# Kernel optimization log

Measured on AMD Instinct MI355X. Metric: run time of the kernel, lower is better.

Reference implementation:

```python
import jax, jax.numpy as jnp
import numpy as np

D_MODEL = 1024
N_HEADS = 16
HEAD_DIM = D_MODEL // N_HEADS
B, T_Q, T_CACHE = 2, 2048, 2048


def setup_inputs() -> dict:
    key = jax.random.key(0)
    ks = jax.random.split(key, 12)
    s = 1.0 / np.sqrt(D_MODEL)
    return {
        "x": jax.random.normal(ks[0], (B, T_Q, D_MODEL), jnp.float32),
        "k_cache": jax.random.normal(ks[1], (B, N_HEADS, T_CACHE, HEAD_DIM), jnp.float32),
        "v_cache": jax.random.normal(ks[2], (B, N_HEADS, T_CACHE, HEAD_DIM), jnp.float32),
        "Wq": jax.random.normal(ks[3], (D_MODEL, D_MODEL), jnp.float32) * s,
        "bq": jax.random.normal(ks[4], (D_MODEL,), jnp.float32) * s,
        "Wk": jax.random.normal(ks[5], (D_MODEL, D_MODEL), jnp.float32) * s,
        "bk": jax.random.normal(ks[6], (D_MODEL,), jnp.float32) * s,
        "Wv": jax.random.normal(ks[7], (D_MODEL, D_MODEL), jnp.float32) * s,
        "bv": jax.random.normal(ks[8], (D_MODEL,), jnp.float32) * s,
        "Wo": jax.random.normal(ks[9], (D_MODEL, D_MODEL), jnp.float32) * s,
        "bo": jax.random.normal(ks[10], (D_MODEL,), jnp.float32) * s,
    }


def reference(x, k_cache, v_cache, Wq, bq, Wk, bk, Wv, bv, Wo, bo):
    B_, T, C = x.shape
    H, Dh = N_HEADS, HEAD_DIM
    scale = Dh ** -0.5

    def proj(W, b):
        # [B,T,C] -> [B,H,T,Dh]
        y = jnp.einsum('btc,cd->btd', x, W) + b
        return y.reshape(B_, T, H, Dh).transpose(0, 2, 1, 3)

    q = proj(Wq, bq)
    k = jnp.concatenate([k_cache, proj(Wk, bk)], axis=2)
    v = jnp.concatenate([v_cache, proj(Wv, bv)], axis=2)

    Tq, Tk = q.shape[2], k.shape[2]
    scores = jnp.einsum('bhqd,bhkd->bhqk', q, k) * scale  # [B,H,Tq,Tk]
    # causal: query i attends to keys j <= i + (Tk - Tq)
    i = jnp.arange(Tq)[:, None]
    j = jnp.arange(Tk)[None, :]
    mask = j > i + (Tk - Tq)
    scores = jnp.where(mask, -jnp.inf, scores)
    attn = jax.nn.softmax(scores, axis=-1)
    out = jnp.einsum('bhqk,bhkd->bhqd', attn, v)
    out = out.transpose(0, 2, 1, 3).reshape(B_, T, C)
    out = jnp.einsum('btc,cd->btd', out, Wo) + bo
    return out, (k, v)
```

## Files before the change

### kernel.cpp

```cpp
#include <hip/hip_runtime.h>
#include <hip/hip_bf16.h>
#include <cstdint>
#include <cstddef>

#define DM 1024
#define NH 16
#define DH 64
#define BB 2
#define TQ 2048
#define TCACHE 2048
#define TKTOT 4096
#define MROWS 4096

typedef __attribute__((ext_vector_type(8))) short bf16x8;
typedef __attribute__((ext_vector_type(4))) short bf16x4;
typedef __attribute__((ext_vector_type(4))) float f32x4;
typedef __attribute__((ext_vector_type(16))) float f32x16;

__device__ __forceinline__ unsigned pk2(float a, float b) {
  unsigned r;
  asm("v_cvt_pk_bf16_f32 %0, %1, %2" : "=v"(r) : "v"(a), "v"(b));
  return r;
}

__device__ __forceinline__ short f2bf(float f) {
  return (short)(unsigned short)pk2(f, f);
}

__device__ __forceinline__ uint2 pk4(float x, float y, float z, float w) {
  uint2 r;
  r.x = pk2(x, y);
  r.y = pk2(z, w);
  return r;
}

__device__ __forceinline__ float bf2f(short s) {
  union { unsigned u; float f; } v;
  v.u = ((unsigned)(unsigned short)s) << 16;
  return v.f;
}

__device__ __forceinline__ float exp2fast(float x) {
#if __has_builtin(__builtin_amdgcn_exp2f)
  return __builtin_amdgcn_exp2f(x);
#else
  return exp2f(x);
#endif
}

__device__ __forceinline__ void plswap(unsigned& a, unsigned& b) {
  asm volatile("v_permlane32_swap_b32 %0, %1" : "+v"(a), "+v"(b));
}

__device__ __forceinline__ void gld_lds16(const short* g, short* l) {
  __builtin_amdgcn_global_load_lds(
      (const __attribute__((address_space(1))) void*)((uintptr_t)g),
      (__attribute__((address_space(3))) void*)((uintptr_t)l), 16, 0, 0);
}

__global__ __launch_bounds__(256) void k_prep(
    const float* __restrict__ x, short* __restrict__ xb,
    const float* __restrict__ W0, const float* __restrict__ W1,
    const float* __restrict__ W2, const float* __restrict__ W3,
    short* __restrict__ Wt,
    const float* __restrict__ kc, short* __restrict__ Kb,
    const float* __restrict__ vc, short* __restrict__ Vtb) {
  __shared__ short lds[64 * 65];
  const int bid = (int)blockIdx.x;
  if (bid < 4096) {
    const size_t i = (size_t)bid * 256 + threadIdx.x;
    const float4 v = ((const float4*)x)[i];
    *(uint2*)(((short4*)xb) + i) = pk4(v.x, v.y, v.z, v.w);
  } else if (bid < 8192) {
    const int local = bid - 4096;
    const int bx = local & 31, by = (local >> 5) & 31, bz = local >> 10;
    short (*tile)[33] = (short(*)[33])lds;
    const float* W = (bz == 0) ? W0 : (bz == 1) ? W1 : (bz == 2) ? W2 : W3;
    short* dst = Wt + (size_t)bz * DM * DM;
    const int k0 = by * 32, n0 = bx * 32;
    const int tx = threadIdx.x & 31, ty = threadIdx.x >> 5;
#pragma unroll
    for (int r = 0; r < 4; r++) {
      const int k = ty + r * 8;
      tile[k][tx] = f2bf(W[(size_t)(k0 + k) * DM + n0 + tx]);
    }
    __syncthreads();
#pragma unroll
    for (int r = 0; r < 4; r++) {
      const int n = ty + r * 8;
      dst[(size_t)(n0 + n) * DM + k0 + tx] = tile[tx][n];
    }
  } else if (bid < 12288) {
    const size_t i = (size_t)(bid - 8192) * 256 + threadIdx.x;
    const float4 v = ((const float4*)kc)[i];
    const size_t e = i * 4;
    const int dh = (int)(e & 63);
    const int t = (int)((e >> 6) & 2047);
    const int bh = (int)(e >> 17);
    *(uint2*)(Kb + ((size_t)bh * TKTOT + t) * DH + dh) = pk4(v.x, v.y, v.z, v.w);
  } else {
    const int local = bid - 12288;
    const int bh = local >> 5;
    const int t0 = (local & 31) * 64;
    short (*tile)[65] = (short(*)[65])lds;
    const int tx = threadIdx.x & 15, ty = threadIdx.x >> 4;
    const float* src = vc + ((size_t)bh * TCACHE + t0) * DH;
#pragma unroll
    for (int r = 0; r < 4; r++) {
      const int t = ty + r * 16;
      const float4 v = *(const float4*)(src + (size_t)t * DH + tx * 4);
      tile[tx * 4 + 0][t] = f2bf(v.x);
      tile[tx * 4 + 1][t] = f2bf(v.y);
      tile[tx * 4 + 2][t] = f2bf(v.z);
      tile[tx * 4 + 3][t] = f2bf(v.w);
    }
    __syncthreads();
    short* vt = Vtb + (size_t)bh * DH * TKTOT + t0;
#pragma unroll
    for (int r = 0; r < 4; r++) {
      const int dh = ty + r * 16;
      short4 o;
      o.x = tile[dh][tx * 4 + 0];
      o.y = tile[dh][tx * 4 + 1];
      o.z = tile[dh][tx * 4 + 2];
      o.w = tile[dh][tx * 4 + 3];
      *(short4*)(vt + (size_t)dh * TKTOT + tx * 4) = o;
    }
  }
}

__global__ __launch_bounds__(256) void k_gemm(
    const short* __restrict__ A, const short* __restrict__ Bt,
    const float* __restrict__ b0, const float* __restrict__ b1, const float* __restrict__ b2,
    const int is_qkv, float* __restrict__ fdst,
    short* __restrict__ Qb, short* __restrict__ Kb, short* __restrict__ Vtb) {
  const int z = is_qkv ? (int)blockIdx.z : 3;
  const short* Bz = Bt + (is_qkv ? (size_t)z * DM * DM : 0);
  const float* bias = (z == 0 || z == 3) ? b0 : (z == 1 ? b1 : b2);

  __shared__ short sA[2][128 * 32];
  __shared__ short sB[2][128 * 32];

  const int m0 = blockIdx.y * 128;
  const int n0 = blockIdx.x * 128;
  const int tid = threadIdx.x;
  const int wv = tid >> 6;
  const int lane = tid & 63;
  const int quad = lane >> 4;
  const int l16 = lane & 15;
  const int wm = (wv >> 1) * 64;
  const int wn = (wv & 1) * 64;

  const f32x4 zero = {0.f, 0.f, 0.f, 0.f};
  f32x4 acc[4][4];
#pragma unroll
  for (int i = 0; i < 4; i++)
#pragma unroll
    for (int j = 0; j < 4; j++) acc[i][j] = zero;

  const int sw = (quad ^ ((l16 >> 1) & 3)) << 4;
  const int afo = (wm + l16) * 64 + sw;
  const int bfo = (wn + l16) * 64 + sw;

#define STAGEG(k0_, b_)                                                         \
  do {                                                                          \
    _Pragma("unroll") for (int s = 0; s < 2; s++) {                             \
      const int c = tid + s * 256;                                              \
      const int row = c >> 2, cs = c & 3;                                       \
      const int gc = cs ^ ((row >> 1) & 3);                                     \
      gld_lds16(A + (size_t)(m0 + row) * DM + (k0_) + gc * 8, &sA[b_][c * 8]);  \
      gld_lds16(Bz + (size_t)(n0 + row) * DM + (k0_) + gc * 8, &sB[b_][c * 8]); \
    }                                                                           \
  } while (0)

  STAGEG(0, 0);
  __syncthreads();
  int buf = 0;
  for (int k0 = 0; k0 < DM; k0 += 32) {
    if (k0 + 32 < DM) STAGEG(k0 + 32, buf ^ 1);
    const char* Ab = (const char*)&sA[0][0] + buf * 8192;
    const char* Bb = (const char*)&sB[0][0] + buf * 8192;
    bf16x8 af[4], bfv[4];
#pragma unroll
    for (int i = 0; i < 4; i++) af[i] = *(const bf16x8*)(Ab + afo + i * 1024);
#pragma unroll
    for (int j = 0; j < 4; j++) bfv[j] = *(const bf16x8*)(Bb + bfo + j * 1024);
    __builtin_amdgcn_s_setprio(1);
#pragma unroll
    for (int i = 0; i < 4; i++)
#pragma unroll
      for (int j = 0; j < 4; j++)
        acc[i][j] = __builtin_amdgcn_mfma_f32_16x16x32_bf16(af[i], bfv[j], acc[i][j], 0, 0, 0);
    __builtin_amdgcn_s_setprio(0);
    __syncthreads();
    buf ^= 1;
  }
#undef STAGEG

#pragma unroll
  for (int i = 0; i < 4; i++) {
#pragma unroll
    for (int j = 0; j < 4; j++) {
      const int gn = n0 + wn + j * 16 + l16;
      const float bb = bias[gn];
#pragma unroll
      for (int r = 0; r < 4; r++) {
        const int gm = m0 + wm + i * 16 + quad * 4 + r;
        const float v = acc[i][j][r] + bb;
        if (z == 3) {
          fdst[(size_t)gm * DM + gn] = v;
        } else {
          const int b_ = gm >> 11, t = gm & 2047;
          const int h_ = gn >> 6, dh = gn & 63;
          if (z == 0) {
            Qb[(((size_t)(b_ * NH + h_)) * TQ + t) * DH + dh] = f2bf(v * 0.18033688011f);
          } else if (z == 1) {
            Kb[(((size_t)(b_ * NH + h_)) * TKTOT + TCACHE + t) * DH + dh] = f2bf(v);
          } else {
            Vtb[(((size_t)(b_ * NH + h_)) * DH + dh) * TKTOT + TCACHE + t] = f2bf(v);
          }
        }
      }
    }
  }
}

__global__ __launch_bounds__(256, 4) void k_attn(const short* __restrict__ Qb,
                                                 const short* __restrict__ Kb,
                                                 const short* __restrict__ Vtb,
                                                 float* __restrict__ Opart,
                                                 float* __restrict__ Lpart) {
  __shared__ short sK[2][64 * 64];
  __shared__ short sV[2][64 * 64];

  const int split = (int)blockIdx.x;
  const int qx = 15 - (int)blockIdx.y;
  const int bh = (int)blockIdx.z;
  const int q0 = qx * 128;
  const int tid = threadIdx.x;
  const int wq = tid >> 6;
  const int lane = tid & 63;
  const int l32 = lane & 31;
  const int h = lane >> 5;

  const int nkt = 2 * qx + 34;
  const int kt0 = (nkt * split) >> 2;
  const int kt1 = (nkt * (split + 1)) >> 2;

  const short* Kg = Kb + (size_t)bh * TKTOT * DH;
  const short* Vtg = Vtb + (size_t)bh * DH * TKTOT;

  const int c0 = tid, c1 = tid + 256;
  const int r0 = c0 >> 3, g0 = ((c0 & 7) ^ (r0 & 7)) * 8;
  const int r1 = c1 >> 3, g1 = ((c1 & 7) ^ (r1 & 7)) * 8;
  const short* Kst0 = Kg + (size_t)r0 * DH + g0;
  const short* Kst1 = Kg + (size_t)r1 * DH + g1;
  const short* Vst0 = Vtg + (size_t)r0 * TKTOT + g0;
  const short* Vst1 = Vtg + (size_t)r1 * TKTOT + g1;

  const short* Qrow = Qb + ((size_t)bh * TQ + q0 + wq * 32 + l32) * DH;
  bf16x8 qf[4];
#pragma unroll
  for (int s = 0; s < 4; s++) qf[s] = *(const bf16x8*)(Qrow + s * 16 + h * 8);

  const char* sKc = (const char*)&sK[0][0];
  const char* sVc = (const char*)&sV[0][0];
  const int rx7 = l32 & 7;
  const int base0 = l32 * 128;
  const int base1 = base0 + 4096;
  int co[4];
#pragma unroll
  for (int ks = 0; ks < 4; ks++) co[ks] = ((2 * ks + h) ^ rx7) << 4;

  const f32x16 zerov = {0, 0, 0, 0, 0, 0, 0, 0, 0, 0, 0, 0, 0, 0, 0, 0};
  f32x16 of0 = zerov;
  f32x16 of1 = zerov;
  float la = 0.f, lb = 0.f, lc = 0.f, ld = 0.f;

#define STAGE(t_, b_)                               \
  do {                                              \
    const size_t koff = (size_t)(t_) * 64 * DH;     \
    const size_t voff = (size_t)(t_) * 64;          \
    short* dK = &sK[b_][0];                         \
    short* dV = &sV[b_][0];                         \
    gld_lds16(Kst0 + koff, dK + c0 * 8);            \
    gld_lds16(Kst1 + koff, dK + c1 * 8);            \
    gld_lds16(Vst0 + voff, dV + c0 * 8);            \
    gld_lds16(Vst1 + voff, dV + c1 * 8);            \
  } while (0)

  STAGE(kt0, 0);
  __syncthreads();
  int buf = 0;

  for (int t = kt0; t < kt1; t++) {
    if (t + 1 < kt1) STAGE(t + 1, buf ^ 1);
    const char* kb_ = sKc + buf * 8192;
    const char* vb_ = sVc + buf * 8192;

    f32x16 sacc0, sacc1;
    __builtin_amdgcn_s_setprio(1);
    {
      const bf16x8 kf0 = *(const bf16x8*)(kb_ + base0 + co[0]);
      const bf16x8 kf1 = *(const bf16x8*)(kb_ + base1 + co[0]);
      sacc0 = __builtin_amdgcn_mfma_f32_32x32x16_bf16(kf0, qf[0], zerov, 0, 0, 0);
      sacc1 = __builtin_amdgcn_mfma_f32_32x32x16_bf16(kf1, qf[0], zerov, 0, 0, 0);
    }
#pragma unroll
    for (int ks = 1; ks < 4; ks++) {
      const bf16x8 kf0 = *(const bf16x8*)(kb_ + base0 + co[ks]);
      const bf16x8 kf1 = *(const bf16x8*)(kb_ + base1 + co[ks]);
      sacc0 = __builtin_amdgcn_mfma_f32_32x32x16_bf16(kf0, qf[ks], sacc0, 0, 0, 0);
      sacc1 = __builtin_amdgcn_mfma_f32_32x32x16_bf16(kf1, qf[ks], sacc1, 0, 0, 0);
    }
    __builtin_amdgcn_s_setprio(0);

    if (t >= nkt - 2) {
      const int qgl = q0 + wq * 32 + l32 + TCACHE;
      const int kb0 = t * 64 + 4 * h;
#pragma unroll
      for (int r = 0; r < 16; r++) {
        const int key = kb0 + (r & 3) + 8 * (r >> 2);
        if (key > qgl) sacc0[r] = -1e30f;
        if (key + 32 > qgl) sacc1[r] = -1e30f;
      }
    }
#pragma unroll
    for (int r = 0; r < 16; r++) {
      const float e0 = exp2fast(sacc0[r]);
      const float e1 = exp2fast(sacc1[r]);
      sacc0[r] = e0;
      sacc1[r] = e1;
      if ((r & 3) == 0) la += e0 + e1;
      else if ((r & 3) == 1) lb += e0 + e1;
      else if ((r & 3) == 2) lc += e0 + e1;
      else ld += e0 + e1;
    }

    bf16x8 pa[4];
#pragma unroll
    for (int s = 0; s < 4; s++) {
      const int o = (s & 1) * 8;
      unsigned w0, w1, w2, w3;
      if (s < 2) {
        w0 = pk2(sacc0[o + 0], sacc0[o + 1]);
        w1 = pk2(sacc0[o + 2], sacc0[o + 3]);
        w2 = pk2(sacc0[o + 4], sacc0[o + 5]);
        w3 = pk2(sacc0[o + 6], sacc0[o + 7]);
      } else {
        w0 = pk2(sacc1[o + 0], sacc1[o + 1]);
        w1 = pk2(sacc1[o + 2], sacc1[o + 3]);
        w2 = pk2(sacc1[o + 4], sacc1[o + 5]);
        w3 = pk2(sacc1[o + 6], sacc1[o + 7]);
      }
      plswap(w0, w2);
      plswap(w1, w3);
      union { unsigned u[4]; bf16x8 v; } pu;
      pu.u[0] = w0; pu.u[1] = w1; pu.u[2] = w2; pu.u[3] = w3;
      pa[s] = pu.v;
    }

    __builtin_amdgcn_s_setprio(1);
#pragma unroll
    for (int ks = 0; ks < 4; ks++) {
      const bf16x8 vf0 = *(const bf16x8*)(vb_ + base0 + co[ks]);
      const bf16x8 vf1 = *(const bf16x8*)(vb_ + base1 + co[ks]);
      of0 = __builtin_amdgcn_mfma_f32_32x32x16_bf16(pa[ks], vf0, of0, 0, 0, 0);
      of1 = __builtin_amdgcn_mfma_f32_32x32x16_bf16(pa[ks], vf1, of1, 0, 0, 0);
    }
    __builtin_amdgcn_s_setprio(0);
    __syncthreads();
    buf ^= 1;
  }
#undef STAGE

  const int pid = (bh * 16 + qx) * 4 + split;
  float* Op = Opart + (size_t)pid * 8192;
#pragma unroll
  for (int r = 0; r < 16; r++) {
    const int ql = wq * 32 + (r & 3) + 8 * (r >> 2) + 4 * h;
    Op[ql * 64 + l32] = of0[r];
    Op[ql * 64 + 32 + l32] = of1[r];
  }
  const float l_lane = (la + lb) + (lc + ld);
  const float l_tot = l_lane + __shfl_xor(l_lane, 32);
  if (h == 0) Lpart[(size_t)pid * 128 + wq * 32 + l32] = l_tot;
}

__global__ __launch_bounds__(256) void k_reduce(const float* __restrict__ Opart,
                                                const float* __restrict__ Lpart,
                                                short* __restrict__ AOb) {
  const int qx = (int)blockIdx.x, bh = (int)blockIdx.y;
  const int b = bh >> 4, hd = bh & 15;
  const int qxb = qx >> 1, hf = qx & 1;
  const int pid = (bh * 16 + qxb) * 4;
  const float* Ob = Opart + (size_t)pid * 8192 + hf * 4096;
  const int t = threadIdx.x;
  const int r_ = t >> 2, c4 = t & 3;
  float l = 0.f;
#pragma unroll
  for (int s = 0; s < 4; s++) l += Lpart[(size_t)(pid + s) * 128 + hf * 64 + r_];
  const float inv = 1.f / l;
  short* dst = AOb + ((size_t)(b * TQ + qx * 64 + r_)) * DM + hd * 64 + c4 * 16;
#pragma unroll
  for (int u = 0; u < 4; u++) {
    const int off = r_ * 64 + c4 * 16 + u * 4;
    float4 a = *(const float4*)(Ob + off);
#pragma unroll
    for (int s = 1; s < 4; s++) {
      const float4 v = *(const float4*)(Ob + (size_t)s * 8192 + off);
      a.x += v.x; a.y += v.y; a.z += v.z; a.w += v.w;
    }
    *(uint2*)(dst + u * 4) = pk4(a.x * inv, a.y * inv, a.z * inv, a.w * inv);
  }
}

__global__ __launch_bounds__(256) void k_expand(const float* __restrict__ kc,
                                                const short* __restrict__ Kb,
                                                float* __restrict__ kF,
                                                const float* __restrict__ vc,
                                                const short* __restrict__ Vtb,
                                                float* __restrict__ vF) {
  __shared__ short tile[64 * 72];
  const int bid = (int)blockIdx.x;
  if (bid < 8192) {
    const size_t f4 = (size_t)bid * 256 + threadIdx.x;
    const size_t e = f4 * 4;
    const int t = (int)((e >> 6) & 4095);
    float4 v;
    if (t < TCACHE) {
      const int dh = (int)(e & 63);
      const int bh = (int)(e >> 18);
      v = *(const float4*)(kc + ((size_t)(bh * TCACHE + t)) * DH + dh);
    } else {
      const short4 s = *(const short4*)(Kb + e);
      v.x = bf2f(s.x); v.y = bf2f(s.y); v.z = bf2f(s.z); v.w = bf2f(s.w);
    }
    *(float4*)(kF + e) = v;
  } else {
    const int local = bid - 8192;
    const int tt = local & 63, bh = local >> 6;
    if (tt < 32) {
#pragma unroll
      for (int k2 = 0; k2 < 4; k2++) {
        const int f = threadIdx.x + k2 * 256;
        const int trow = f >> 4, dh4 = f & 15;
        const size_t si = ((size_t)(bh * TCACHE) + tt * 64 + trow) * DH + dh4 * 4;
        const size_t di = ((size_t)(bh * TKTOT) + tt * 64 + trow) * DH + dh4 * 4;
        *(float4*)(vF + di) = *(const float4*)(vc + si);
      }
    } else {
      const int t0 = tt * 64;
#pragma unroll
      for (int k2 = 0; k2 < 4; k2++) {
        const int f = threadIdx.x + k2 * 256;
        const int dh = f >> 4, tc4 = f & 15;
        const short4 s = *(const short4*)(Vtb + ((size_t)(bh * DH + dh)) * TKTOT + t0 + tc4 * 4);
        *(short4*)(&tile[dh * 72 + tc4 * 4]) = s;
      }
      __syncthreads();
#pragma unroll
      for (int k2 = 0; k2 < 4; k2++) {
        const int f = threadIdx.x + k2 * 256;
        const int trow = f >> 4, dh4 = f & 15;
        float4 v;
        v.x = bf2f(tile[(dh4 * 4 + 0) * 72 + trow]);
        v.y = bf2f(tile[(dh4 * 4 + 1) * 72 + trow]);
        v.z = bf2f(tile[(dh4 * 4 + 2) * 72 + trow]);
        v.w = bf2f(tile[(dh4 * 4 + 3) * 72 + trow]);
        *(float4*)(vF + ((size_t)(bh * TKTOT) + t0 + trow) * DH + dh4 * 4) = v;
      }
    }
  }
}


extern "C" void kernel_launch(void* const* d_in, const int* in_sizes, int n_in,
                              void* d_out, int out_size, void* d_ws, size_t ws_size,
                              hipStream_t stream) {
  const float* x = (const float*)d_in[0];
  const float* kc = (const float*)d_in[1];
  const float* vc = (const float*)d_in[2];
  const float* Wq = (const float*)d_in[3];
  const float* bq = (const float*)d_in[4];
  const float* Wk = (const float*)d_in[5];
  const float* bk = (const float*)d_in[6];
  const float* Wv = (const float*)d_in[7];
  const float* bv = (const float*)d_in[8];
  const float* Wo = (const float*)d_in[9];
  const float* bo = (const float*)d_in[10];

  float* out = (float*)d_out;
  float* kF = out + (size_t)BB * TQ * DM;
  float* vF = kF + (size_t)BB * NH * TKTOT * DH;
  float* Opart = kF;
  float* Lpart = out;

  char* ws = (char*)d_ws;
  short* xb = (short*)ws;   ws += (size_t)MROWS * DM * 2;
  short* Wt = (short*)ws;   ws += (size_t)4 * DM * DM * 2;
  short* Qb = (short*)ws;   ws += (size_t)BB * NH * TQ * DH * 2;
  short* Kb = (short*)ws;   ws += (size_t)BB * NH * TKTOT * DH * 2;
  short* Vtb = (short*)ws;  ws += (size_t)BB * NH * TKTOT * DH * 2;
  short* AOb = (short*)ws;

  k_prep<<<13312, 256, 0, stream>>>(x, xb, Wq, Wk, Wv, Wo, Wt, kc, Kb, vc, Vtb);
  k_gemm<<<dim3(DM / 128, MROWS / 128, 3), 256, 0, stream>>>(
      xb, Wt, bq, bk, bv, 1, nullptr, Qb, Kb, Vtb);
  k_attn<<<dim3(4, 16, 32), 256, 0, stream>>>(Qb, Kb, Vtb, Opart, Lpart);
  k_reduce<<<dim3(32, 32), 256, 0, stream>>>(Opart, Lpart, AOb);
  k_expand<<<10240, 256, 0, stream>>>(kc, Kb, kF, vc, Vtb, vF);
  k_gemm<<<dim3(DM / 128, MROWS / 128, 1), 256, 0, stream>>>(
      AOb, Wt + (size_t)3 * DM * DM, bo, bo, bo, 0, out, nullptr, nullptr, nullptr);
}
```

Baseline: 317.0 us.

## Fuse attention, reduction and KV expansion into one kernel without split-K

Removes the 4-way key split of the attention kernel, so each block handles all key tiles for its query tile and normalizes and writes bf16 output directly. This drops the partial-output buffers and the separate reduce kernel. The KV-cache fp32 expansion is merged into the same launch as extra blocks that can fill idle CUs while long attention blocks run. Attention blocks are ordered to interleave long and short causal tiles. The trade-off is fewer, longer attention blocks (512 instead of 2048), which raises tail imbalance risk in exchange for one fewer launch and less partial-sum traffic.

```diff
diff --git a/kernel.cpp b/kernel.cpp
--- a/kernel.cpp
+++ b/kernel.cpp
@@ -225,206 +225,170 @@
   }
 }
 
-__global__ __launch_bounds__(256, 4) void k_attn(const short* __restrict__ Qb,
-                                                 const short* __restrict__ Kb,
-                                                 const short* __restrict__ Vtb,
-                                                 float* __restrict__ Opart,
-                                                 float* __restrict__ Lpart) {
-  __shared__ short sK[2][64 * 64];
-  __shared__ short sV[2][64 * 64];
-
-  const int split = (int)blockIdx.x;
-  const int qx = 15 - (int)blockIdx.y;
-  const int bh = (int)blockIdx.z;
-  const int q0 = qx * 128;
-  const int tid = threadIdx.x;
-  const int wq = tid >> 6;
-  const int lane = tid & 63;
-  const int l32 = lane & 31;
-  const int h = lane >> 5;
-
-  const int nkt = 2 * qx + 34;
-  const int kt0 = (nkt * split) >> 2;
-  const int kt1 = (nkt * (split + 1)) >> 2;
-
-  const short* Kg = Kb + (size_t)bh * TKTOT * DH;
-  const short* Vtg = Vtb + (size_t)bh * DH * TKTOT;
-
-  const int c0 = tid, c1 = tid + 256;
-  const int r0 = c0 >> 3, g0 = ((c0 & 7) ^ (r0 & 7)) * 8;
-  const int r1 = c1 >> 3, g1 = ((c1 & 7) ^ (r1 & 7)) * 8;
-  const short* Kst0 = Kg + (size_t)r0 * DH + g0;
-  const short* Kst1 = Kg + (size_t)r1 * DH + g1;
-  const short* Vst0 = Vtg + (size_t)r0 * TKTOT + g0;
-  const short* Vst1 = Vtg + (size_t)r1 * TKTOT + g1;
-
-  const short* Qrow = Qb + ((size_t)bh * TQ + q0 + wq * 32 + l32) * DH;
-  bf16x8 qf[4];
-#pragma unroll
-  for (int s = 0; s < 4; s++) qf[s] = *(const bf16x8*)(Qrow + s * 16 + h * 8);
-
-  const char* sKc = (const char*)&sK[0][0];
-  const char* sVc = (const char*)&sV[0][0];
-  const int rx7 = l32 & 7;
-  const int base0 = l32 * 128;
-  const int base1 = base0 + 4096;
-  int co[4];
-#pragma unroll
-  for (int ks = 0; ks < 4; ks++) co[ks] = ((2 * ks + h) ^ rx7) << 4;
-
-  const f32x16 zerov = {0, 0, 0, 0, 0, 0, 0, 0, 0, 0, 0, 0, 0, 0, 0, 0};
-  f32x16 of0 = zerov;
-  f32x16 of1 = zerov;
-  float la = 0.f, lb = 0.f, lc = 0.f, ld = 0.f;
-
-#define STAGE(t_, b_)                               \
-  do {                                              \
-    const size_t koff = (size_t)(t_) * 64 * DH;     \
-    const size_t voff = (size_t)(t_) * 64;          \
-    short* dK = &sK[b_][0];                         \
-    short* dV = &sV[b_][0];                         \
-    gld_lds16(Kst0 + koff, dK + c0 * 8);            \
-    gld_lds16(Kst1 + koff, dK + c1 * 8);            \
-    gld_lds16(Vst0 + voff, dV + c0 * 8);            \
-    gld_lds16(Vst1 + voff, dV + c1 * 8);            \
-  } while (0)
-
-  STAGE(kt0, 0);
-  __syncthreads();
-  int buf = 0;
-
-  for (int t = kt0; t < kt1; t++) {
-    if (t + 1 < kt1) STAGE(t + 1, buf ^ 1);
-    const char* kb_ = sKc + buf * 8192;
-    const char* vb_ = sVc + buf * 8192;
-
-    f32x16 sacc0, sacc1;
-    __builtin_amdgcn_s_setprio(1);
-    {
-      const bf16x8 kf0 = *(const bf16x8*)(kb_ + base0 + co[0]);
-      const bf16x8 kf1 = *(const bf16x8*)(kb_ + base1 + co[0]);
-      sacc0 = __builtin_amdgcn_mfma_f32_32x32x16_bf16(kf0, qf[0], zerov, 0, 0, 0);
-      sacc1 = __builtin_amdgcn_mfma_f32_32x32x16_bf16(kf1, qf[0], zerov, 0, 0, 0);
-    }
-#pragma unroll
-    for (int ks = 1; ks < 4; ks++) {
-      const bf16x8 kf0 = *(const bf16x8*)(kb_ + base0 + co[ks]);
-      const bf16x8 kf1 = *(const bf16x8*)(kb_ + base1 + co[ks]);
-      sacc0 = __builtin_amdgcn_mfma_f32_32x32x16_bf16(kf0, qf[ks], sacc0, 0, 0, 0);
-      sacc1 = __builtin_amdgcn_mfma_f32_32x32x16_bf16(kf1, qf[ks], sacc1, 0, 0, 0);
-    }
-    __builtin_amdgcn_s_setprio(0);
-
-    if (t >= nkt - 2) {
-      const int qgl = q0 + wq * 32 + l32 + TCACHE;
-      const int kb0 = t * 64 + 4 * h;
+__global__ __launch_bounds__(256, 4) void k_attn_expand(
+    const short* __restrict__ Qb, const short* __restrict__ Kb,
+    const short* __restrict__ Vtb, short* __restrict__ AOb,
+    const float* __restrict__ kc, float* __restrict__ kF,
+    const float* __restrict__ vc, float* __restrict__ vF) {
+  __shared__ short SH[16384];
+
+  const int bid = (int)blockIdx.x;
+  if (bid < 512) {
+    const int y = bid >> 5;
+    const int bh = bid & 31;
+    const int qx = (y < 8) ? (15 - y) : (y - 8);
+    const int q0 = qx * 128;
+    const int tid = threadIdx.x;
+    const int wq = tid >> 6;
+    const int lane = tid & 63;
+    const int l32 = lane & 31;
+    const int h = lane >> 5;
+
+    const int nkt = 2 * qx + 34;
+
+    const short* Kg = Kb + (size_t)bh * TKTOT * DH;
+    const short* Vtg = Vtb + (size_t)bh * DH * TKTOT;
+
+    const int c0 = tid, c1 = tid + 256;
+    const int r0 = c0 >> 3, g0 = ((c0 & 7) ^ (r0 & 7)) * 8;
+    const int r1 = c1 >> 3, g1 = ((c1 & 7) ^ (r1 & 7)) * 8;
+    const short* Kst0 = Kg + (size_t)r0 * DH + g0;
+    const short* Kst1 = Kg + (size_t)r1 * DH + g1;
+    const short* Vst0 = Vtg + (size_t)r0 * TKTOT + g0;
+    const short* Vst1 = Vtg + (size_t)r1 * TKTOT + g1;
+
+    const short* Qrow = Qb + ((size_t)bh * TQ + q0 + wq * 32 + l32) * DH;
+    bf16x8 qf[4];
+#pragma unroll
+    for (int s = 0; s < 4; s++) qf[s] = *(const bf16x8*)(Qrow + s * 16 + h * 8);
+
+    const char* sKc = (const char*)SH;
+    const char* sVc = (const char*)SH + 16384;
+    const int rx7 = l32 & 7;
+    const int base0 = l32 * 128;
+    const int base1 = base0 + 4096;
+    int co[4];
+#pragma unroll
+    for (int ks = 0; ks < 4; ks++) co[ks] = ((2 * ks + h) ^ rx7) << 4;
+
+    const f32x16 zerov = {0, 0, 0, 0, 0, 0, 0, 0, 0, 0, 0, 0, 0, 0, 0, 0};
+    f32x16 of0 = zerov;
+    f32x16 of1 = zerov;
+    float la = 0.f, lb = 0.f, lc = 0.f, ld = 0.f;
+
+#define STAGE(t_, b_)                                    \
+    do {                                                 \
+      const size_t koff = (size_t)(t_) * 64 * DH;        \
+      const size_t voff = (size_t)(t_) * 64;             \
+      short* dK = SH + (b_)*4096;                        \
+      short* dV = SH + 8192 + (b_)*4096;                 \
+      gld_lds16(Kst0 + koff, dK + c0 * 8);               \
+      gld_lds16(Kst1 + koff, dK + c1 * 8);               \
+      gld_lds16(Vst0 + voff, dV + c0 * 8);               \
+      gld_lds16(Vst1 + voff, dV + c1 * 8);               \
+    } while (0)
+
+    STAGE(0, 0);
+    __syncthreads();
+    int buf = 0;
+
+    for (int t = 0; t < nkt; t++) {
+      if (t + 1 < nkt) STAGE(t + 1, buf ^ 1);
+      const char* kb_ = sKc + buf * 8192;
+      const char* vb_ = sVc + buf * 8192;
+
+      f32x16 sacc0, sacc1;
+      __builtin_amdgcn_s_setprio(1);
+      {
+        const bf16x8 kf0 = *(const bf16x8*)(kb_ + base0 + co[0]);
+        const bf16x8 kf1 = *(const bf16x8*)(kb_ + base1 + co[0]);
+        sacc0 = __builtin_amdgcn_mfma_f32_32x32x16_bf16(kf0, qf[0], zerov, 0, 0, 0);
+        sacc1 = __builtin_amdgcn_mfma_f32_32x32x16_bf16(kf1, qf[0], zerov, 0, 0, 0);
+      }
+#pragma unroll
+      for (int ks = 1; ks < 4; ks++) {
+        const bf16x8 kf0 = *(const bf16x8*)(kb_ + base0 + co[ks]);
+        const bf16x8 kf1 = *(const bf16x8*)(kb_ + base1 + co[ks]);
+        sacc0 = __builtin_amdgcn_mfma_f32_32x32x16_bf16(kf0, qf[ks], sacc0, 0, 0, 0);
+        sacc1 = __builtin_amdgcn_mfma_f32_32x32x16_bf16(kf1, qf[ks], sacc1, 0, 0, 0);
+      }
+      __builtin_amdgcn_s_setprio(0);
+
+      if (t >= nkt - 2) {
+        const int qgl = q0 + wq * 32 + l32 + TCACHE;
+        const int kb0 = t * 64 + 4 * h;
+#pragma unroll
+        for (int r = 0; r < 16; r++) {
+          const int key = kb0 + (r & 3) + 8 * (r >> 2);
+          if (key > qgl) sacc0[r] = -1e30f;
+          if (key + 32 > qgl) sacc1[r] = -1e30f;
+        }
+      }
 #pragma unroll
       for (int r = 0; r < 16; r++) {
-        const int key = kb0 + (r & 3) + 8 * (r >> 2);
-        if (key > qgl) sacc0[r] = -1e30f;
-        if (key + 32 > qgl) sacc1[r] = -1e30f;
-      }
-    }
+        const float e0 = exp2fast(sacc0[r]);
+        const float e1 = exp2fast(sacc1[r]);
+        sacc0[r] = e0;
+        sacc1[r] = e1;
+        if ((r & 3) == 0) la += e0 + e1;
+        else if ((r & 3) == 1) lb += e0 + e1;
+        else if ((r & 3) == 2) lc += e0 + e1;
+        else ld += e0 + e1;
+      }
+
+      bf16x8 pa[4];
+#pragma unroll
+      for (int s = 0; s < 4; s++) {
+        const int o = (s & 1) * 8;
+        unsigned w0, w1, w2, w3;
+        if (s < 2) {
+          w0 = pk2(sacc0[o + 0], sacc0[o + 1]);
+          w1 = pk2(sacc0[o + 2], sacc0[o + 3]);
+          w2 = pk2(sacc0[o + 4], sacc0[o + 5]);
+          w3 = pk2(sacc0[o + 6], sacc0[o + 7]);
+        } else {
+          w0 = pk2(sacc1[o + 0], sacc1[o + 1]);
+          w1 = pk2(sacc1[o + 2], sacc1[o + 3]);
+          w2 = pk2(sacc1[o + 4], sacc1[o + 5]);
+          w3 = pk2(sacc1[o + 6], sacc1[o + 7]);
+        }
+        plswap(w0, w2);
+        plswap(w1, w3);
+        union { unsigned u[4]; bf16x8 v; } pu;
+        pu.u[0] = w0; pu.u[1] = w1; pu.u[2] = w2; pu.u[3] = w3;
+        pa[s] = pu.v;
+      }
+
+      __builtin_amdgcn_s_setprio(1);
+#pragma unroll
+      for (int ks = 0; ks < 4; ks++) {
+        const bf16x8 vf0 = *(const bf16x8*)(vb_ + base0 + co[ks]);
+        const bf16x8 vf1 = *(const bf16x8*)(vb_ + base1 + co[ks]);
+        of0 = __builtin_amdgcn_mfma_f32_32x32x16_bf16(pa[ks], vf0, of0, 0, 0, 0);
+        of1 = __builtin_amdgcn_mfma_f32_32x32x16_bf16(pa[ks], vf1, of1, 0, 0, 0);
+      }
+      __builtin_amdgcn_s_setprio(0);
+      __syncthreads();
+      buf ^= 1;
+    }
+#undef STAGE
+
+    float* sLf = (float*)SH;
+    const float l_lane = (la + lb) + (lc + ld);
+    const float l_tot = l_lane + __shfl_xor(l_lane, 32);
+    if (h == 0) sLf[wq * 32 + l32] = l_tot;
+    const int b_ = bh >> 4, h_ = bh & 15;
 #pragma unroll
     for (int r = 0; r < 16; r++) {
-      const float e0 = exp2fast(sacc0[r]);
-      const float e1 = exp2fast(sacc1[r]);
-      sacc0[r] = e0;
-      sacc1[r] = e1;
-      if ((r & 3) == 0) la += e0 + e1;
-      else if ((r & 3) == 1) lb += e0 + e1;
-      else if ((r & 3) == 2) lc += e0 + e1;
-      else ld += e0 + e1;
-    }
-
-    bf16x8 pa[4];
-#pragma unroll
-    for (int s = 0; s < 4; s++) {
-      const int o = (s & 1) * 8;
-      unsigned w0, w1, w2, w3;
-      if (s < 2) {
-        w0 = pk2(sacc0[o + 0], sacc0[o + 1]);
-        w1 = pk2(sacc0[o + 2], sacc0[o + 3]);
-        w2 = pk2(sacc0[o + 4], sacc0[o + 5]);
-        w3 = pk2(sacc0[o + 6], sacc0[o + 7]);
-      } else {
-        w0 = pk2(sacc1[o + 0], sacc1[o + 1]);
-        w1 = pk2(sacc1[o + 2], sacc1[o + 3]);
-        w2 = pk2(sacc1[o + 4], sacc1[o + 5]);
-        w3 = pk2(sacc1[o + 6], sacc1[o + 7]);
-      }
-      plswap(w0, w2);
-      plswap(w1, w3);
-      union { unsigned u[4]; bf16x8 v; } pu;
-      pu.u[0] = w0; pu.u[1] = w1; pu.u[2] = w2; pu.u[3] = w3;
-      pa[s] = pu.v;
-    }
-
-    __builtin_amdgcn_s_setprio(1);
-#pragma unroll
-    for (int ks = 0; ks < 4; ks++) {
-      const bf16x8 vf0 = *(const bf16x8*)(vb_ + base0 + co[ks]);
-      const bf16x8 vf1 = *(const bf16x8*)(vb_ + base1 + co[ks]);
-      of0 = __builtin_amdgcn_mfma_f32_32x32x16_bf16(pa[ks], vf0, of0, 0, 0, 0);
-      of1 = __builtin_amdgcn_mfma_f32_32x32x16_bf16(pa[ks], vf1, of1, 0, 0, 0);
-    }
-    __builtin_amdgcn_s_setprio(0);
-    __syncthreads();
-    buf ^= 1;
-  }
-#undef STAGE
-
-  const int pid = (bh * 16 + qx) * 4 + split;
-  float* Op = Opart + (size_t)pid * 8192;
-#pragma unroll
-  for (int r = 0; r < 16; r++) {
-    const int ql = wq * 32 + (r & 3) + 8 * (r >> 2) + 4 * h;
-    Op[ql * 64 + l32] = of0[r];
-    Op[ql * 64 + 32 + l32] = of1[r];
-  }
-  const float l_lane = (la + lb) + (lc + ld);
-  const float l_tot = l_lane + __shfl_xor(l_lane, 32);
-  if (h == 0) Lpart[(size_t)pid * 128 + wq * 32 + l32] = l_tot;
-}
-
-__global__ __launch_bounds__(256) void k_reduce(const float* __restrict__ Opart,
-                                                const float* __restrict__ Lpart,
-                                                short* __restrict__ AOb) {
-  const int qx = (int)blockIdx.x, bh = (int)blockIdx.y;
-  const int b = bh >> 4, hd = bh & 15;
-  const int qxb = qx >> 1, hf = qx & 1;
-  const int pid = (bh * 16 + qxb) * 4;
-  const float* Ob = Opart + (size_t)pid * 8192 + hf * 4096;
-  const int t = threadIdx.x;
-  const int r_ = t >> 2, c4 = t & 3;
-  float l = 0.f;
-#pragma unroll
-  for (int s = 0; s < 4; s++) l += Lpart[(size_t)(pid + s) * 128 + hf * 64 + r_];
-  const float inv = 1.f / l;
-  short* dst = AOb + ((size_t)(b * TQ + qx * 64 + r_)) * DM + hd * 64 + c4 * 16;
-#pragma unroll
-  for (int u = 0; u < 4; u++) {
-    const int off = r_ * 64 + c4 * 16 + u * 4;
-    float4 a = *(const float4*)(Ob + off);
-#pragma unroll
-    for (int s = 1; s < 4; s++) {
-      const float4 v = *(const float4*)(Ob + (size_t)s * 8192 + off);
-      a.x += v.x; a.y += v.y; a.z += v.z; a.w += v.w;
-    }
-    *(uint2*)(dst + u * 4) = pk4(a.x * inv, a.y * inv, a.z * inv, a.w * inv);
-  }
-}
-
-__global__ __launch_bounds__(256) void k_expand(const float* __restrict__ kc,
-                                                const short* __restrict__ Kb,
-                                                float* __restrict__ kF,
-                                                const float* __restrict__ vc,
-                                                const short* __restrict__ Vtb,
-                                                float* __restrict__ vF) {
-  __shared__ short tile[64 * 72];
-  const int bid = (int)blockIdx.x;
-  if (bid < 8192) {
-    const size_t f4 = (size_t)bid * 256 + threadIdx.x;
+      const int row = (r & 3) + 8 * (r >> 2) + 4 * h;
+      const float inv = 1.f / sLf[wq * 32 + row];
+      const int qg = q0 + wq * 32 + row;
+      short* d = AOb + ((size_t)(b_ * TQ + qg)) * DM + h_ * 64;
+      d[l32] = f2bf(of0[r] * inv);
+      d[32 + l32] = f2bf(of1[r] * inv);
+    }
+  } else if (bid < 8704) {
+    const size_t f4 = (size_t)(bid - 512) * 256 + threadIdx.x;
     const size_t e = f4 * 4;
     const int t = (int)((e >> 6) & 4095);
     float4 v;
@@ -438,8 +402,9 @@
     }
     *(float4*)(kF + e) = v;
   } else {
-    const int local = bid - 8192;
+    const int local = bid - 8704;
     const int tt = local & 63, bh = local >> 6;
+    short* tile = SH;
     if (tt < 32) {
 #pragma unroll
       for (int k2 = 0; k2 < 4; k2++) {
@@ -493,8 +458,6 @@
   float* out = (float*)d_out;
   float* kF = out + (size_t)BB * TQ * DM;
   float* vF = kF + (size_t)BB * NH * TKTOT * DH;
-  float* Opart = kF;
-  float* Lpart = out;
 
   char* ws = (char*)d_ws;
   short* xb = (short*)ws;   ws += (size_t)MROWS * DM * 2;
@@ -507,9 +470,7 @@
   k_prep<<<13312, 256, 0, stream>>>(x, xb, Wq, Wk, Wv, Wo, Wt, kc, Kb, vc, Vtb);
   k_gemm<<<dim3(DM / 128, MROWS / 128, 3), 256, 0, stream>>>(
       xb, Wt, bq, bk, bv, 1, nullptr, Qb, Kb, Vtb);
-  k_attn<<<dim3(4, 16, 32), 256, 0, stream>>>(Qb, Kb, Vtb, Opart, Lpart);
-  k_reduce<<<dim3(32, 32), 256, 0, stream>>>(Opart, Lpart, AOb);
-  k_expand<<<10240, 256, 0, stream>>>(kc, Kb, kF, vc, Vtb, vF);
+  k_attn_expand<<<10752, 256, 0, stream>>>(Qb, Kb, Vtb, AOb, kc, kF, vc, vF);
   k_gemm<<<dim3(DM / 128, MROWS / 128, 1), 256, 0, stream>>>(
       AOb, Wt + (size_t)3 * DM * DM, bo, bo, bo, 0, out, nullptr, nullptr, nullptr);
 }
```

New measurement: 271.0 us. -14.5%, faster.
